# Kernel tuning notes

Measured on AMD Instinct MI355X. Metric: run time of the kernel, lower is better.

Reference implementation:

```python
import jax, jax.numpy as jnp
import numpy as np

NUM_HEADS = 16
HEAD_DIM = 128


def apply_rope(x, rope):
    # x: [B, H, N, D]; rope: [N, 1, D]
    freqs = rope[:, 0, :]  # [N, D]
    cos = jnp.repeat(freqs[:, 0::2], 2, axis=-1)[None, None]  # [1,1,N,D]
    sin = jnp.repeat(freqs[:, 1::2], 2, axis=-1)[None, None]
    xr = x.reshape(*x.shape[:-1], -1, 2)
    x_real, x_imag = xr[..., 0], xr[..., 1]
    x_rot = jnp.stack([-x_imag, x_real], axis=-1).reshape(x.shape)
    return (x * cos + x_rot * sin).astype(x.dtype)


def setup_inputs() -> dict:
    key = jax.random.key(0)
    k1, k2, k3, k4 = jax.random.split(key, 4)
    B, N, hidden = 2, 2048, 2048
    x = jax.random.normal(k1, (B, N, hidden), dtype=jnp.float32)
    rope = jax.random.uniform(k2, (N, 1, HEAD_DIM), dtype=jnp.float32)
    qkv_w = jax.random.normal(k3, (hidden, 3 * NUM_HEADS * HEAD_DIM), dtype=jnp.float32) * 0.02
    out_w = jax.random.normal(k4, (NUM_HEADS * HEAD_DIM, hidden), dtype=jnp.float32) * 0.02
    return {"x": x, "rope": rope, "qkv_w": qkv_w, "out_w": out_w}


def reference(x, rope, qkv_w, out_w):
    B, N, _ = x.shape
    H, D = NUM_HEADS, HEAD_DIM
    qkv = (x @ qkv_w).reshape(B, N, 3, H, D)  # [B,N,3,H,D]
    q = jnp.transpose(qkv[:, :, 0], (0, 2, 1, 3))  # [B,H,N,D]
    k = jnp.transpose(qkv[:, :, 1], (0, 2, 1, 3))
    v = jnp.transpose(qkv[:, :, 2], (0, 2, 1, 3))
    q = apply_rope(q, rope)
    k = apply_rope(k, rope)
    scale = 1.0 / np.float32(np.sqrt(D))
    scores = jnp.einsum('bhqd,bhkd->bhqk', q, k) * scale
    attn = jax.nn.softmax(scores, axis=-1)
    out = jnp.einsum('bhqk,bhkd->bhqd', attn, v)
    out = jnp.transpose(out, (0, 2, 1, 3)).reshape(B, N, H * D)
    return out @ out_w
```

## Files before the change

kernel.cpp:

```cpp
#include <hip/hip_runtime.h>
#include <stdint.h>


typedef unsigned short u16;
typedef __bf16 bf16x8 __attribute__((ext_vector_type(8)));
typedef float f32x4 __attribute__((ext_vector_type(4)));

#define DI static __device__ __forceinline__

DI u16 f2b(float f) {
  union { float f; unsigned u; } v; v.f = f;
  unsigned r = v.u + 0x7FFFu + ((v.u >> 16) & 1u);
  return (u16)(r >> 16);
}

#if __has_builtin(__builtin_amdgcn_exp2f)
DI float EXP2(float x) { return __builtin_amdgcn_exp2f(x); }
#else
DI float EXP2(float x) { return exp2f(x); }
#endif

typedef unsigned int __attribute__((address_space(1))) *gas1_t;
typedef unsigned int __attribute__((address_space(3))) *las3_t;

DI void async16(const void* g, void* l) {
  __builtin_amdgcn_global_load_lds((gas1_t)g, (las3_t)l, 16, 0, 0);
}

DI bf16x8 ldsv(const u16* p) { return *(const bf16x8*)p; }

__global__ void k_cvt(const float* __restrict__ in, u16* __restrict__ out, int n4) {
  int i = blockIdx.x * blockDim.x + threadIdx.x;
  if (i >= n4) return;
  float4 v = ((const float4*)in)[i];
  ushort4 o;
  o.x = f2b(v.x); o.y = f2b(v.y); o.z = f2b(v.z); o.w = f2b(v.w);
  ((ushort4*)out)[i] = o;
}

__global__ void k_tcvt(const float* __restrict__ in, u16* __restrict__ out, int R, int C) {
  __shared__ float t[32][33];
  int bx = blockIdx.x * 32, by = blockIdx.y * 32;
  int tx = threadIdx.x, ty = threadIdx.y;
#pragma unroll
  for (int i = 0; i < 4; i++)
    t[ty + i * 8][tx] = in[(size_t)(by + ty + i * 8) * C + bx + tx];
  __syncthreads();
#pragma unroll
  for (int i = 0; i < 4; i++)
    out[(size_t)(bx + ty + i * 8) * R + by + tx] = f2b(t[tx][ty + i * 8]);
}

template <int MODE>
__global__ __launch_bounds__(256) void k_gemm(
    const u16* __restrict__ A, const u16* __restrict__ BT, const int K,
    float* __restrict__ C, const int ldc,
    const float* __restrict__ rope,
    u16* __restrict__ Qp, u16* __restrict__ Kp, u16* __restrict__ VTp) {
  __shared__ u16 As[8192];
  __shared__ u16 Bs[8192];
  const int tid = threadIdx.x;
  const int w = tid >> 6, lane = tid & 63;
  const int g = lane >> 4, lr = lane & 15;
  const int wm = (w >> 1) << 6, wn = (w & 1) << 6;
  const int bm0 = blockIdx.y << 7, bn0 = blockIdx.x << 7;

  const int cg8 = (lane & 7) ^ (lane >> 3);
  const int row_l = lane >> 3;

  const u16* Ag = A + (size_t)(bm0 + (w << 5) + row_l) * K + (cg8 << 3);
  const u16* Bg = BT + (size_t)(bn0 + (w << 5) + row_l) * K + (cg8 << 3);
  u16* Asd = As + (w << 11);
  u16* Bsd = Bs + (w << 11);
  const size_t rstep = (size_t)K << 3;

  const f32x4 zf = {0.f, 0.f, 0.f, 0.f};
  f32x4 acc[4][4];
#pragma unroll
  for (int i = 0; i < 4; i++)
#pragma unroll
    for (int j = 0; j < 4; j++) acc[i][j] = zf;

  for (int kt = 0; kt < K; kt += 64) {
#pragma unroll
    for (int i = 0; i < 4; i++) {
      async16(Ag + (size_t)i * rstep + kt, Asd + (i << 9));
      async16(Bg + (size_t)i * rstep + kt, Bsd + (i << 9));
    }
    __syncthreads();
#pragma unroll
    for (int kk = 0; kk < 2; kk++) {
      bf16x8 af[4], bf[4];
      const int swz = ((((kk << 2) + g) ^ (lr & 7)) << 3);
#pragma unroll
      for (int i = 0; i < 4; i++) {
        af[i] = ldsv(As + ((wm + (i << 4) + lr) << 6) + swz);
        bf[i] = ldsv(Bs + ((wn + (i << 4) + lr) << 6) + swz);
      }
#pragma unroll
      for (int i = 0; i < 4; i++)
#pragma unroll
        for (int j = 0; j < 4; j++)
          acc[i][j] = __builtin_amdgcn_mfma_f32_16x16x32_bf16(af[i], bf[j], acc[i][j], 0, 0, 0);
    }
    __syncthreads();
  }

  if constexpr (MODE == 0) {
#pragma unroll
    for (int i = 0; i < 4; i++) {
      const int row0 = bm0 + wm + (i << 4) + (g << 2);
#pragma unroll
      for (int j = 0; j < 4; j++) {
        const int col = bn0 + wn + (j << 4) + lr;
#pragma unroll
        for (int e = 0; e < 4; e++)
          C[(size_t)(row0 + e) * ldc + col] = acc[i][j][e];
      }
    }
  } else {
    const int sidx = bn0 >> 11;
    const int h = (bn0 >> 7) & 15;
    const int b = bm0 >> 11;
    const int nb = (bm0 & 2047) + wm;
    if (sidx < 2) {
      u16* dst = (sidx == 0 ? Qp : Kp) + ((size_t)(b * 16 + h) << 18);
      const float qs = (sidx == 0) ? 0.08838834764831845f * 1.4426950408889634f : 1.0f;
#pragma unroll
      for (int i = 0; i < 4; i++) {
#pragma unroll
        for (int j = 0; j < 4; j++) {
          const int d = wn + (j << 4) + lr;
          const float sg = (d & 1) ? 1.f : -1.f;
          const int dpe = d & ~1, dpo = d | 1;
#pragma unroll
          for (int e = 0; e < 4; e++) {
            const int n = nb + (i << 4) + (g << 2) + e;
            const float v = acc[i][j][e];
            const float p = __shfl_xor(v, 1);
            const float cf = rope[(n << 7) + dpe];
            const float sf = rope[(n << 7) + dpo];
            dst[((size_t)n << 7) + d] = f2b((v * cf + sg * p * sf) * qs);
          }
        }
      }
    } else {
      u16* dst = VTp + ((size_t)(b * 16 + h) << 18);
#pragma unroll
      for (int i = 0; i < 4; i++) {
#pragma unroll
        for (int j = 0; j < 4; j++) {
          const int d = wn + (j << 4) + lr;
          const int n0 = nb + (i << 4) + (g << 2);
          ushort4 o;
          o.x = f2b(acc[i][j][0]); o.y = f2b(acc[i][j][1]);
          o.z = f2b(acc[i][j][2]); o.w = f2b(acc[i][j][3]);
          *(ushort4*)(dst + ((size_t)d << 11) + n0) = o;
        }
      }
    }
  }
}

__global__ __launch_bounds__(256, 2) void k_attn(
    const u16* __restrict__ Q, const u16* __restrict__ Kt,
    const u16* __restrict__ VT, u16* __restrict__ Og) {
  __shared__ u16 Ks[8192];
  __shared__ u16 Vs[8192];
  __shared__ u16 Pb[4][2048];
  const int tid = threadIdx.x;
  const int w = tid >> 6, lane = tid & 63;
  const int g = lane >> 4, lr = lane & 15;
  const int wgid = ((blockIdx.x & 7) << 6) + (blockIdx.x >> 3);
  const int qt = wgid & 15, h = (wgid >> 4) & 15, b = wgid >> 8;
  const size_t bh = (size_t)(b * 16 + h) << 18;
  const u16* Qb = Q + bh;
  const u16* Kb = Kt + bh;
  const u16* Vb = VT + bh;
  u16* Pw = &Pb[w][0];

  const int qr0 = (qt << 7) + (w << 5);
  bf16x8 qf[2][4];
#pragma unroll
  for (int mi = 0; mi < 2; mi++)
#pragma unroll
    for (int kk = 0; kk < 4; kk++)
      qf[mi][kk] = *(const bf16x8*)(Qb + ((size_t)(qr0 + (mi << 4) + lr) << 7) + (kk << 5) + (g << 3));

  const int krow_l = lane >> 4;
  const int kcg_base = lane & 15;
  const int vrow_l = lane >> 3;
  const int vcg_base = lane & 7;

  auto stageK = [&](int kt) {
#pragma unroll
    for (int i = 0; i < 4; i++) {
      const int grp = (w << 2) + i;
      const int row = (grp << 2) + krow_l;
      const int cg = kcg_base ^ (row & 7);
      async16(Kb + ((size_t)((kt << 6) + row) << 7) + (cg << 3), Ks + (grp << 9));
    }
  };
  auto stageV = [&](int kt) {
#pragma unroll
    for (int i = 0; i < 4; i++) {
      const int grp = (w << 2) + i;
      const int d = (grp << 3) + vrow_l;
      const int cg = vcg_base ^ (d & 7);
      async16(Vb + ((size_t)d << 11) + (kt << 6) + (cg << 3), Vs + (grp << 9));
    }
  };

  const f32x4 zf = {0.f, 0.f, 0.f, 0.f};
  f32x4 o[2][8];
  float m_[2][4], l_[2][4];
#pragma unroll
  for (int mi = 0; mi < 2; mi++) {
#pragma unroll
    for (int ni = 0; ni < 8; ni++) o[mi][ni] = zf;
#pragma unroll
    for (int e = 0; e < 4; e++) { m_[mi][e] = -1.0e30f; l_[mi][e] = 0.f; }
  }

  stageK(0);
  stageV(0);
  __syncthreads();

  for (int kt = 0; kt < 32; kt++) {
    f32x4 s[2][4];
#pragma unroll
    for (int mi = 0; mi < 2; mi++)
#pragma unroll
      for (int ni = 0; ni < 4; ni++) s[mi][ni] = zf;
#pragma unroll
    for (int kk = 0; kk < 4; kk++) {
      bf16x8 kf[4];
#pragma unroll
      for (int ni = 0; ni < 4; ni++) {
        const int row = (ni << 4) + lr;
        kf[ni] = ldsv(Ks + (row << 7) + ((((kk << 2) + g) ^ (row & 7)) << 3));
      }
      __builtin_amdgcn_s_setprio(1);
#pragma unroll
      for (int mi = 0; mi < 2; mi++)
#pragma unroll
        for (int ni = 0; ni < 4; ni++)
          s[mi][ni] = __builtin_amdgcn_mfma_f32_16x16x32_bf16(qf[mi][kk], kf[ni], s[mi][ni], 0, 0, 0);
      __builtin_amdgcn_s_setprio(0);
    }

    float pm[2][4];
#pragma unroll
    for (int mi = 0; mi < 2; mi++)
#pragma unroll
      for (int e = 0; e < 4; e++) {
        float v = fmaxf(fmaxf(s[mi][0][e], s[mi][1][e]), fmaxf(s[mi][2][e], s[mi][3][e]));
        v = fmaxf(v, __shfl_xor(v, 1));
        v = fmaxf(v, __shfl_xor(v, 2));
        v = fmaxf(v, __shfl_xor(v, 4));
        v = fmaxf(v, __shfl_xor(v, 8));
        pm[mi][e] = v;
      }
    bool need = false;
#pragma unroll
    for (int mi = 0; mi < 2; mi++)
#pragma unroll
      for (int e = 0; e < 4; e++) need = need || (pm[mi][e] > m_[mi][e] + 8.0f);
    if (__any(need)) {
      float al[2][4];
#pragma unroll
      for (int mi = 0; mi < 2; mi++)
#pragma unroll
        for (int e = 0; e < 4; e++) {
          const float mn = fmaxf(m_[mi][e], pm[mi][e]);
          const float a = EXP2(m_[mi][e] - mn);
          m_[mi][e] = mn;
          l_[mi][e] *= a;
          al[mi][e] = a;
        }
#pragma unroll
      for (int mi = 0; mi < 2; mi++)
#pragma unroll
        for (int ni = 0; ni < 8; ni++)
#pragma unroll
          for (int e = 0; e < 4; e++) o[mi][ni][e] *= al[mi][e];
    }
    float ps[2][4];
#pragma unroll
    for (int mi = 0; mi < 2; mi++)
#pragma unroll
      for (int e = 0; e < 4; e++) ps[mi][e] = 0.f;
#pragma unroll
    for (int mi = 0; mi < 2; mi++)
#pragma unroll
      for (int ni = 0; ni < 4; ni++)
#pragma unroll
        for (int e = 0; e < 4; e++) {
          const float p = EXP2(s[mi][ni][e] - m_[mi][e]);
          s[mi][ni][e] = p;
          ps[mi][e] += p;
        }
#pragma unroll
    for (int mi = 0; mi < 2; mi++)
#pragma unroll
      for (int e = 0; e < 4; e++) {
        float t = ps[mi][e];
        t += __shfl_xor(t, 1);
        t += __shfl_xor(t, 2);
        t += __shfl_xor(t, 4);
        t += __shfl_xor(t, 8);
        l_[mi][e] += t;
      }
#pragma unroll
    for (int mi = 0; mi < 2; mi++)
#pragma unroll
      for (int ni = 0; ni < 4; ni++)
#pragma unroll
        for (int e = 0; e < 4; e++) {
          const int row = (mi << 4) + (g << 2) + e;
          const int col = (ni << 4) + lr;
          Pw[(row << 6) + (((col >> 3) ^ (row & 7)) << 3) + (col & 7)] = f2b(s[mi][ni][e]);
        }

    __syncthreads();
    if (kt < 31) stageK(kt + 1);

#pragma unroll
    for (int kk = 0; kk < 2; kk++) {
      bf16x8 pf[2];
#pragma unroll
      for (int mi = 0; mi < 2; mi++) {
        const int row = (mi << 4) + lr;
        pf[mi] = ldsv(Pw + (row << 6) + ((((kk << 2) + g) ^ (row & 7)) << 3));
      }
      bf16x8 vf[8];
#pragma unroll
      for (int ni = 0; ni < 8; ni++) {
        const int d = (ni << 4) + lr;
        vf[ni] = ldsv(Vs + (d << 6) + ((((kk << 2) + g) ^ (d & 7)) << 3));
      }
      __builtin_amdgcn_s_setprio(1);
#pragma unroll
      for (int mi = 0; mi < 2; mi++)
#pragma unroll
        for (int ni = 0; ni < 8; ni++)
          o[mi][ni] = __builtin_amdgcn_mfma_f32_16x16x32_bf16(pf[mi], vf[ni], o[mi][ni], 0, 0, 0);
      __builtin_amdgcn_s_setprio(0);
    }

    __syncthreads();
    if (kt < 31) stageV(kt + 1);
  }

  u16* Ob = Og + ((size_t)b << 22) + (h << 7);
#pragma unroll
  for (int mi = 0; mi < 2; mi++) {
    float inv[4];
#pragma unroll
    for (int e = 0; e < 4; e++) inv[e] = 1.0f / l_[mi][e];
#pragma unroll
    for (int ni = 0; ni < 8; ni++) {
      const int d = (ni << 4) + lr;
#pragma unroll
      for (int e = 0; e < 4; e++) {
        const int n = qr0 + (mi << 4) + (g << 2) + e;
        Ob[((size_t)n << 11) + d] = f2b(o[mi][ni][e] * inv[e]);
      }
    }
  }
}

extern "C" void kernel_launch(void* const* d_in, const int* in_sizes, int n_in,
                              void* d_out, int out_size, void* d_ws, size_t ws_size,
                              hipStream_t stream) {
  const float* x = (const float*)d_in[0];
  const float* rope = (const float*)d_in[1];
  const float* qkv_w = (const float*)d_in[2];
  const float* out_w = (const float*)d_in[3];
  float* out = (float*)d_out;

  char* ws = (char*)d_ws;
  u16* xb    = (u16*)(ws);
  u16* wqkvT = (u16*)(ws + 16777216);
  u16* woT   = (u16*)(ws + 41943040);
  u16* Qp    = (u16*)(ws + 50331648);
  u16* Kp    = (u16*)(ws + 67108864);
  u16* VTp   = (u16*)(ws + 83886080);
  u16* Og    = xb;

  k_cvt<<<8192, 256, 0, stream>>>(x, xb, 2097152);
  k_tcvt<<<dim3(192, 64), dim3(32, 8), 0, stream>>>(qkv_w, wqkvT, 2048, 6144);
  k_tcvt<<<dim3(64, 64), dim3(32, 8), 0, stream>>>(out_w, woT, 2048, 2048);
  k_gemm<1><<<dim3(48, 32), 256, 0, stream>>>(xb, wqkvT, 2048, nullptr, 0, rope, Qp, Kp, VTp);
  k_attn<<<512, 256, 0, stream>>>(Qp, Kp, VTp, Og);
  k_gemm<0><<<dim3(16, 32), 256, 0, stream>>>(Og, woT, 2048, out, 2048, nullptr, nullptr, nullptr, nullptr);
}
```

Baseline: 442.0 us.

## Rewrite QKV projection GEMM with 256x256 tiles and triple-buffered async loads

Replaces the templated 128x128 QKV GEMM with a dedicated 512-thread kernel that computes 256x256 output tiles. It uses a three-stage LDS ring filled with async global-to-LDS copies, splits the MFMA work into two halves interleaved with B-fragment loads and barriers, raises wave priority around the MFMA blocks, and remaps block IDs across XCDs. The goal is more data reuse per loaded tile and better overlap of memory and compute. The cost is much higher register and LDS pressure, and the grid shrinks to 384 blocks.

```diff
diff --git a/kernel.cpp b/kernel.cpp
--- a/kernel.cpp
+++ b/kernel.cpp
@@ -51,12 +51,9 @@
     out[(size_t)(bx + ty + i * 8) * R + by + tx] = f2b(t[tx][ty + i * 8]);
 }
 
-template <int MODE>
-__global__ __launch_bounds__(256) void k_gemm(
+__global__ __launch_bounds__(256) void k_gemm0(
     const u16* __restrict__ A, const u16* __restrict__ BT, const int K,
-    float* __restrict__ C, const int ldc,
-    const float* __restrict__ rope,
-    u16* __restrict__ Qp, u16* __restrict__ Kp, u16* __restrict__ VTp) {
+    float* __restrict__ C, const int ldc) {
   __shared__ u16 As[8192];
   __shared__ u16 Bs[8192];
   const int tid = threadIdx.x;
@@ -106,57 +103,149 @@
     __syncthreads();
   }
 
-  if constexpr (MODE == 0) {
-#pragma unroll
-    for (int i = 0; i < 4; i++) {
-      const int row0 = bm0 + wm + (i << 4) + (g << 2);
-#pragma unroll
-      for (int j = 0; j < 4; j++) {
-        const int col = bn0 + wn + (j << 4) + lr;
-#pragma unroll
-        for (int e = 0; e < 4; e++)
-          C[(size_t)(row0 + e) * ldc + col] = acc[i][j][e];
+#pragma unroll
+  for (int i = 0; i < 4; i++) {
+    const int row0 = bm0 + wm + (i << 4) + (g << 2);
+#pragma unroll
+    for (int j = 0; j < 4; j++) {
+      const int col = bn0 + wn + (j << 4) + lr;
+#pragma unroll
+      for (int e = 0; e < 4; e++)
+        C[(size_t)(row0 + e) * ldc + col] = acc[i][j][e];
+    }
+  }
+}
+
+__global__ __launch_bounds__(512, 2) void k_gemm256(
+    const u16* __restrict__ A, const u16* __restrict__ BT,
+    const float* __restrict__ rope,
+    u16* __restrict__ Qp, u16* __restrict__ Kp, u16* __restrict__ VTp) {
+  constexpr int K = 2048;
+  constexpr int NT = 64;
+  __shared__ u16 SA[3][8192];
+  __shared__ u16 SB[3][8192];
+  const int tid = threadIdx.x;
+  const int w = tid >> 6, lane = tid & 63;
+  const int g = lane >> 4, lr = lane & 15;
+  const int wm_w = (w >> 2) << 7;
+  const int wn_w = (w & 3) << 6;
+
+  const int wgid = ((blockIdx.x & 7) * 48) + (blockIdx.x >> 3);
+  const int nt = wgid >> 4, mt = wgid & 15;
+  const int bm0 = mt << 8, bn0 = nt << 8;
+
+  const int r0 = (w << 4) + (lane >> 2);
+  const int c0 = (lane & 3) ^ ((lane >> 3) & 3);
+  const u16* Ap = A + (size_t)(bm0 + r0) * K + (c0 << 3);
+  const u16* Bp = BT + (size_t)(bn0 + r0) * K + (c0 << 3);
+  const size_t half = (size_t)K << 7;
+  const int ldso = w << 9;
+
+  auto stageA = [&](u16* sa, int t2) {
+    const size_t kc = (size_t)t2 << 5;
+    async16(Ap + kc, sa + ldso);
+    async16(Ap + half + kc, sa + 4096 + ldso);
+  };
+  auto stageB = [&](u16* sb, int t2) {
+    const size_t kc = (size_t)t2 << 5;
+    async16(Bp + kc, sb + ldso);
+    async16(Bp + half + kc, sb + 4096 + ldso);
+  };
+
+  f32x4 acc[8][4] = {};
+  bf16x8 af[8], bf[4];
+  u16 *aR = SA[0], *aF = SA[1], *aS = SA[2];
+  u16 *bR = SB[0], *bF = SB[1], *bS = SB[2];
+
+  stageA(aR, 0); stageB(bR, 0);
+  stageA(aF, 1); stageB(bF, 1);
+  asm volatile("s_waitcnt vmcnt(4)" ::: "memory");
+  __builtin_amdgcn_s_barrier();
+  __builtin_amdgcn_sched_barrier(0);
+
+  const int rsw = ((g ^ ((lr >> 1) & 3)) << 3);
+
+  for (int t = 0; t < NT; ++t) {
+#pragma unroll
+    for (int i = 0; i < 8; i++)
+      af[i] = ldsv(aR + ((wm_w + (i << 4) + lr) << 5) + rsw);
+#pragma unroll
+    for (int j = 0; j < 2; j++)
+      bf[j] = ldsv(bR + ((wn_w + (j << 4) + lr) << 5) + rsw);
+    if (t < NT - 2) stageA(aS, t + 2);
+    __builtin_amdgcn_s_barrier();
+    __builtin_amdgcn_sched_barrier(0);
+    __builtin_amdgcn_s_setprio(1);
+#pragma unroll
+    for (int i = 0; i < 8; i++)
+#pragma unroll
+      for (int j = 0; j < 2; j++)
+        acc[i][j] = __builtin_amdgcn_mfma_f32_16x16x32_bf16(af[i], bf[j], acc[i][j], 0, 0, 0);
+    __builtin_amdgcn_s_setprio(0);
+    __builtin_amdgcn_s_barrier();
+    __builtin_amdgcn_sched_barrier(0);
+#pragma unroll
+    for (int j = 2; j < 4; j++)
+      bf[j] = ldsv(bR + ((wn_w + (j << 4) + lr) << 5) + rsw);
+    if (t < NT - 2) stageB(bS, t + 2);
+    __builtin_amdgcn_s_barrier();
+    __builtin_amdgcn_sched_barrier(0);
+    __builtin_amdgcn_s_setprio(1);
+#pragma unroll
+    for (int i = 0; i < 8; i++)
+#pragma unroll
+      for (int j = 2; j < 4; j++)
+        acc[i][j] = __builtin_amdgcn_mfma_f32_16x16x32_bf16(af[i], bf[j], acc[i][j], 0, 0, 0);
+    __builtin_amdgcn_s_setprio(0);
+    if (t < NT - 2) asm volatile("s_waitcnt vmcnt(4)" ::: "memory");
+    else            asm volatile("s_waitcnt vmcnt(0)" ::: "memory");
+    __builtin_amdgcn_s_barrier();
+    __builtin_amdgcn_sched_barrier(0);
+    u16* ta = aR; aR = aF; aF = aS; aS = ta;
+    u16* tb = bR; bR = bF; bF = bS; bS = tb;
+  }
+
+  const int sidx = bn0 >> 11;
+  const int b = bm0 >> 11;
+  if (sidx < 2) {
+    u16* base = (sidx == 0) ? Qp : Kp;
+    const float sc = (sidx == 0) ? 0.08838834764831845f * 1.4426950408889634f : 1.0f;
+#pragma unroll
+    for (int j = 0; j < 4; j++) {
+      const int gn = bn0 + wn_w + (j << 4) + lr;
+      const int hh = (gn >> 7) & 15;
+      const int d = gn & 127;
+      const float sg = (d & 1) ? 1.f : -1.f;
+      const int dpe = d & ~1, dpo = d | 1;
+      u16* dst = base + ((size_t)(b * 16 + hh) << 18);
+#pragma unroll
+      for (int i = 0; i < 8; i++) {
+        const int n0 = (bm0 & 2047) + wm_w + (i << 4) + (g << 2);
+#pragma unroll
+        for (int e = 0; e < 4; e++) {
+          const int n = n0 + e;
+          const float v = acc[i][j][e];
+          const float p = __shfl_xor(v, 1);
+          const float cf = rope[(n << 7) + dpe];
+          const float sf = rope[(n << 7) + dpo];
+          dst[((size_t)n << 7) + d] = f2b((v * cf + sg * p * sf) * sc);
+        }
       }
     }
   } else {
-    const int sidx = bn0 >> 11;
-    const int h = (bn0 >> 7) & 15;
-    const int b = bm0 >> 11;
-    const int nb = (bm0 & 2047) + wm;
-    if (sidx < 2) {
-      u16* dst = (sidx == 0 ? Qp : Kp) + ((size_t)(b * 16 + h) << 18);
-      const float qs = (sidx == 0) ? 0.08838834764831845f * 1.4426950408889634f : 1.0f;
-#pragma unroll
-      for (int i = 0; i < 4; i++) {
-#pragma unroll
-        for (int j = 0; j < 4; j++) {
-          const int d = wn + (j << 4) + lr;
-          const float sg = (d & 1) ? 1.f : -1.f;
-          const int dpe = d & ~1, dpo = d | 1;
-#pragma unroll
-          for (int e = 0; e < 4; e++) {
-            const int n = nb + (i << 4) + (g << 2) + e;
-            const float v = acc[i][j][e];
-            const float p = __shfl_xor(v, 1);
-            const float cf = rope[(n << 7) + dpe];
-            const float sf = rope[(n << 7) + dpo];
-            dst[((size_t)n << 7) + d] = f2b((v * cf + sg * p * sf) * qs);
-          }
-        }
-      }
-    } else {
-      u16* dst = VTp + ((size_t)(b * 16 + h) << 18);
-#pragma unroll
-      for (int i = 0; i < 4; i++) {
-#pragma unroll
-        for (int j = 0; j < 4; j++) {
-          const int d = wn + (j << 4) + lr;
-          const int n0 = nb + (i << 4) + (g << 2);
-          ushort4 o;
-          o.x = f2b(acc[i][j][0]); o.y = f2b(acc[i][j][1]);
-          o.z = f2b(acc[i][j][2]); o.w = f2b(acc[i][j][3]);
-          *(ushort4*)(dst + ((size_t)d << 11) + n0) = o;
-        }
+#pragma unroll
+    for (int j = 0; j < 4; j++) {
+      const int gn = bn0 + wn_w + (j << 4) + lr;
+      const int hh = (gn >> 7) & 15;
+      const int d = gn & 127;
+      u16* dst = VTp + ((size_t)(b * 16 + hh) << 18) + ((size_t)d << 11);
+#pragma unroll
+      for (int i = 0; i < 8; i++) {
+        const int n0 = (bm0 & 2047) + wm_w + (i << 4) + (g << 2);
+        ushort4 o;
+        o.x = f2b(acc[i][j][0]); o.y = f2b(acc[i][j][1]);
+        o.z = f2b(acc[i][j][2]); o.w = f2b(acc[i][j][3]);
+        *(ushort4*)(dst + n0) = o;
       }
     }
   }
@@ -391,7 +480,7 @@
   k_cvt<<<8192, 256, 0, stream>>>(x, xb, 2097152);
   k_tcvt<<<dim3(192, 64), dim3(32, 8), 0, stream>>>(qkv_w, wqkvT, 2048, 6144);
   k_tcvt<<<dim3(64, 64), dim3(32, 8), 0, stream>>>(out_w, woT, 2048, 2048);
-  k_gemm<1><<<dim3(48, 32), 256, 0, stream>>>(xb, wqkvT, 2048, nullptr, 0, rope, Qp, Kp, VTp);
+  k_gemm256<<<384, 512, 0, stream>>>(xb, wqkvT, rope, Qp, Kp, VTp);
   k_attn<<<512, 256, 0, stream>>>(Qp, Kp, VTp, Og);
-  k_gemm<0><<<dim3(16, 32), 256, 0, stream>>>(Og, woT, 2048, out, 2048, nullptr, nullptr, nullptr, nullptr);
-}
+  k_gemm0<<<dim3(16, 32), 256, 0, stream>>>(Og, woT, 2048, out, 2048);
+}
```

Result: slower. 463.0 us (+4.7%).
